# Kernel optimization log

Hardware: AMD Instinct MI355X
Metric: run time of the kernel (lower is better)

## Reference

```python
import jax, jax.numpy as jnp
import numpy as np

N, NFEAT, NHID1, NHID2 = 16384, 128, 128, 64

def setup_inputs() -> dict:
    key = jax.random.key(0)
    k1, k2, k3, k4 = jax.random.split(key, 4)
    feature = jax.random.normal(k1, (N, NFEAT), dtype=jnp.float32)
    # dense (row-normalized) adjacency surrogate
    adj = jax.random.uniform(k2, (N, N), dtype=jnp.float32) / N
    W1 = jax.random.normal(k3, (NFEAT, NHID1), dtype=jnp.float32) / np.sqrt(NFEAT)
    b1 = jnp.zeros((NHID1,), dtype=jnp.float32)
    W2 = jax.random.normal(k4, (NHID1, NHID2), dtype=jnp.float32) / np.sqrt(NHID1)
    b2 = jnp.zeros((NHID2,), dtype=jnp.float32)
    return {"feature": feature, "adj": adj, "W1": W1, "b1": b1, "W2": W2, "b2": b2}

def reference(feature, adj, W1, b1, W2, b2):
    # layer 1: support = X@W1; agg = A@support; relu
    h = jax.nn.relu(adj @ (feature @ W1) + b1)
    # dropout is identity in eval mode
    # layer 2
    out = adj @ (h @ W2) + b2
    return out
```

## Files before the change

kernel.cpp:

```cpp
#include <hip/hip_runtime.h>
#include <stdint.h>

typedef float  f32x4  __attribute__((ext_vector_type(4)));
typedef short  short8 __attribute__((ext_vector_type(8)));
typedef __bf16 bf16x8 __attribute__((ext_vector_type(8)));

__device__ __forceinline__ unsigned short f2bf(float f) {
    unsigned u = __builtin_bit_cast(unsigned, f);
    unsigned r = u + 0x7fffu + ((u >> 16) & 1u);
    return (unsigned short)(r >> 16);
}

__device__ __forceinline__ short8 cvt8(f32x4 a, f32x4 b) {
    short8 r;
    r[0] = (short)f2bf(a[0]); r[1] = (short)f2bf(a[1]);
    r[2] = (short)f2bf(a[2]); r[3] = (short)f2bf(a[3]);
    r[4] = (short)f2bf(b[0]); r[5] = (short)f2bf(b[1]);
    r[6] = (short)f2bf(b[2]); r[7] = (short)f2bf(b[3]);
    return r;
}

typedef const __attribute__((address_space(1))) void* gas_p;
typedef __attribute__((address_space(3))) void*       las_p;
__device__ __forceinline__ void gld_lds16(const void* g, void* l) {
    __builtin_amdgcn_global_load_lds((gas_p)g, (las_p)l, 16, 0, 0);
}

__device__ __forceinline__ f32x4 mfma16(short8 a, short8 b, f32x4 c) {
    return __builtin_amdgcn_mfma_f32_16x16x32_bf16(
        __builtin_bit_cast(bf16x8, a), __builtin_bit_cast(bf16x8, b), c, 0, 0, 0);
}

template<int NMAT>
__global__ __launch_bounds__(256) void k_xw_t(const float* __restrict__ X,
                                              const float* __restrict__ W,
                                              short* __restrict__ St, int M) {
    constexpr int K   = 128;
    constexpr int NPT = NMAT / 4;
    __shared__ float Xs[64][129];
    __shared__ float Ws[K][NMAT];

    const int tid = threadIdx.x;
    const int m0  = blockIdx.x * 64;

    constexpr int WCH = K * NMAT / 4 / 256;
    #pragma unroll
    for (int j = 0; j < WCH; ++j) {
        int ch = tid + j * 256;
        ((float4*)Ws)[ch] = ((const float4*)W)[ch];
    }
    #pragma unroll
    for (int j = 0; j < 8; ++j) {
        int ch = tid + j * 256;
        int r = ch >> 5, c4 = ch & 31;
        float4 v = *(const float4*)(X + (size_t)(m0 + r) * K + c4 * 4);
        Xs[r][c4 * 4 + 0] = v.x; Xs[r][c4 * 4 + 1] = v.y;
        Xs[r][c4 * 4 + 2] = v.z; Xs[r][c4 * 4 + 3] = v.w;
    }
    __syncthreads();

    const int m  = tid & 63;
    const int n0 = (tid >> 6) * NPT;
    float acc[NPT];
    #pragma unroll
    for (int i = 0; i < NPT; ++i) acc[i] = 0.f;

    for (int k = 0; k < K; ++k) {
        float x = Xs[m][k];
        #pragma unroll
        for (int i = 0; i < NPT; i += 4) {
            float4 w = *(const float4*)&Ws[k][n0 + i];
            acc[i + 0] += x * w.x; acc[i + 1] += x * w.y;
            acc[i + 2] += x * w.z; acc[i + 3] += x * w.w;
        }
    }
    #pragma unroll
    for (int i = 0; i < NPT; ++i)
        St[(size_t)(n0 + i) * M + m0 + m] = (short)f2bf(acc[i]);
}

template<int BN, bool RELU>
__global__ __launch_bounds__(128, 1) void k_adj_gemm(const float* __restrict__ A,
                                                     const short* __restrict__ Bt,
                                                     const float* __restrict__ bias,
                                                     float* __restrict__ out,
                                                     int M, int K) {
    constexpr int BM    = 32, BK = 64;
    constexpr int NF    = BN / 16;
    constexpr int BTILE = BN * BK * 2;
    constexpr int BCH   = BTILE / (128 * 16);
    constexpr int VMCNT = BCH + 8;

    __shared__ short Bs[2][BN * 64];

    const int tid  = threadIdx.x;
    const int wave = tid >> 6, lane = tid & 63;
    const int lr   = lane & 15, lk = lane >> 4;
    const int row_g = blockIdx.x * BM + wave * 16 + lr;

    const char* Abase = (const char*)A + (size_t)row_g * K * 4 + lk * 32;

    const int offs0 = (lk * 16)        ^ ((lr & 7) << 4);
    const int offs1 = (64 + lk * 16)   ^ ((lr & 7) << 4);

    f32x4 acc[NF];
    #pragma unroll
    for (int n = 0; n < NF; ++n) acc[n] = (f32x4)0.f;

    f32x4 a0[4], a1[4];
    const int NT = K / BK;

#define STAGE_B(BUF, KT)                                                        \
    {                                                                           \
        _Pragma("unroll")                                                       \
        for (int j = 0; j < BCH; ++j) {                                         \
            int o = (tid + j * 128) * 16;          \
            int r = o >> 7, w = o & 127;                                        \
            const char* src = (const char*)Bt + (size_t)r * (K * 2)             \
                              + (size_t)(KT) * 128 + (w ^ ((r & 7) << 4));      \
            gld_lds16(src, (char*)&Bs[BUF][0] + o);                             \
        }                                                                       \
    }

#define LOAD_A(SLOT, KT)                                                        \
    {                                                                           \
        const char* p = Abase + (size_t)(KT) * 256;                             \
        SLOT[0] = *(const f32x4*)(p);                                           \
        SLOT[1] = *(const f32x4*)(p + 16);                                      \
        SLOT[2] = *(const f32x4*)(p + 128);                                     \
        SLOT[3] = *(const f32x4*)(p + 144);                                     \
    }

    LOAD_A(a0, 0)
    STAGE_B(0, 0)
    LOAD_A(a1, 1)

#define ITER(KT, SA, CUR, NXT)                                                  \
    {                                                                           \
               \
        { int ktn = (KT) + 1 < NT ? (KT) + 1 : NT - 1; STAGE_B(NXT, ktn) }      \
        __builtin_amdgcn_sched_barrier(0);                                      \
             \
        short8 fa0 = cvt8(SA[0], SA[1]);                                        \
        short8 fa1 = cvt8(SA[2], SA[3]);                                        \
                                             \
        { int kta = (KT) + 2 < NT ? (KT) + 2 : NT - 1; LOAD_A(SA, kta) }        \
        __builtin_amdgcn_sched_barrier(0);                                      \
                              \
        asm volatile("s_waitcnt vmcnt(%0)" :: "i"(VMCNT) : "memory");           \
        __builtin_amdgcn_s_barrier();                                           \
        __builtin_amdgcn_sched_barrier(0);                                      \
                                      \
        _Pragma("unroll")                                                       \
        for (int n = 0; n < NF; ++n) {                                          \
            short8 b0 = *(const short8*)((const char*)&Bs[CUR][0]               \
                                         + n * 2048 + lr * 128 + offs0);        \
            acc[n] = mfma16(fa0, b0, acc[n]);                                   \
            short8 b1 = *(const short8*)((const char*)&Bs[CUR][0]               \
                                         + n * 2048 + lr * 128 + offs1);        \
            acc[n] = mfma16(fa1, b1, acc[n]);                                   \
        }                                                                       \
        __builtin_amdgcn_sched_barrier(0);                                      \
        __builtin_amdgcn_s_barrier();         \
    }

    for (int g = 0; g < NT / 2; ++g) {
        ITER(2 * g,     a0, 0, 1)
        ITER(2 * g + 1, a1, 1, 0)
    }
#undef ITER
#undef LOAD_A
#undef STAGE_B

    #pragma unroll
    for (int n = 0; n < NF; ++n) {
        int col = n * 16 + lr;
        float bv = bias[col];
        #pragma unroll
        for (int j = 0; j < 4; ++j) {
            int row = blockIdx.x * BM + wave * 16 + lk * 4 + j;
            float v = acc[n][j] + bv;
            if (RELU) v = fmaxf(v, 0.f);
            out[(size_t)row * BN + col] = v;
        }
    }
}

extern "C" void kernel_launch(void* const* d_in, const int* in_sizes, int n_in,
                              void* d_out, int out_size, void* d_ws, size_t ws_size,
                              hipStream_t stream) {
    const int N = 16384, NH1 = 128, NH2 = 64;
    const float* feature = (const float*)d_in[0];
    const float* adj     = (const float*)d_in[1];
    const float* W1      = (const float*)d_in[2];
    const float* b1      = (const float*)d_in[3];
    const float* W2      = (const float*)d_in[4];
    const float* b2      = (const float*)d_in[5];

    short* S1t = (short*)d_ws;
    float* h   = (float*)((char*)d_ws + (4u << 20));
    short* S2t = (short*)((char*)d_ws + (12u << 20));

    k_xw_t<NH1><<<N / 64, 256, 0, stream>>>(feature, W1, S1t, N);
    k_adj_gemm<NH1, true ><<<N / 32, 128, 0, stream>>>(adj, S1t, b1, h, N, N);
    k_xw_t<NH2><<<N / 64, 256, 0, stream>>>(h, W2, S2t, N);
    k_adj_gemm<NH2, false><<<N / 32, 128, 0, stream>>>(adj, S2t, b2, (float*)d_out, N, N);
    (void)in_sizes; (void)n_in; (void)out_size; (void)ws_size;
}
```

Before: 539.1 us.

## Use 64-row blocks with triple-buffered B tiles and one barrier per step

The adjacency GEMM now runs 256-thread blocks covering 64 rows, so each staged B tile is shared by four waves instead of two, which halves B traffic per row. B staging moves to a three-buffer LDS ring. That lets the trailing barrier go, leaving a single barrier per k-step, and the loop is unrolled six ways with a hard-coded trip count. The risks are more LDS per block, occupancy hints that may not hold, and a loop count fixed at K=16384, which breaks other sizes.

Result: no change. 533.5 us (-1.0%).

```diff
diff --git a/kernel.cpp b/kernel.cpp
--- a/kernel.cpp
+++ b/kernel.cpp
@@ -80,28 +80,29 @@
 }
 
 template<int BN, bool RELU>
-__global__ __launch_bounds__(128, 1) void k_adj_gemm(const float* __restrict__ A,
+__global__ __launch_bounds__(256, 2) void k_adj_gemm(const float* __restrict__ A,
                                                      const short* __restrict__ Bt,
                                                      const float* __restrict__ bias,
                                                      float* __restrict__ out,
                                                      int M, int K) {
-    constexpr int BM    = 32, BK = 64;
+    constexpr int BM    = 64, BK = 64;
     constexpr int NF    = BN / 16;
-    constexpr int BTILE = BN * BK * 2;
-    constexpr int BCH   = BTILE / (128 * 16);
-    constexpr int VMCNT = BCH + 8;
-
-    __shared__ short Bs[2][BN * 64];
+    constexpr int BCH   = BN * BK * 2 / (256 * 16);
+    constexpr int VMCNT = BCH + 4;
+
+    __shared__ short Bs[3][BN * 64];
 
     const int tid  = threadIdx.x;
     const int wave = tid >> 6, lane = tid & 63;
     const int lr   = lane & 15, lk = lane >> 4;
-    const int row_g = blockIdx.x * BM + wave * 16 + lr;
+    const int row0 = blockIdx.x * BM;
+    const int row_g = row0 + wave * 16 + lr;
 
     const char* Abase = (const char*)A + (size_t)row_g * K * 4 + lk * 32;
 
-    const int offs0 = (lk * 16)        ^ ((lr & 7) << 4);
-    const int offs1 = (64 + lk * 16)   ^ ((lr & 7) << 4);
+    const int key   = (lr & 7) << 4;
+    const int offs0 = (lk * 16) ^ key;
+    const int offs1 = (64 + lk * 16) ^ key;
 
     f32x4 acc[NF];
     #pragma unroll
@@ -109,18 +110,6 @@
 
     f32x4 a0[4], a1[4];
     const int NT = K / BK;
-
-#define STAGE_B(BUF, KT)                                                        \
-    {                                                                           \
-        _Pragma("unroll")                                                       \
-        for (int j = 0; j < BCH; ++j) {                                         \
-            int o = (tid + j * 128) * 16;          \
-            int r = o >> 7, w = o & 127;                                        \
-            const char* src = (const char*)Bt + (size_t)r * (K * 2)             \
-                              + (size_t)(KT) * 128 + (w ^ ((r & 7) << 4));      \
-            gld_lds16(src, (char*)&Bs[BUF][0] + o);                             \
-        }                                                                       \
-    }
 
 #define LOAD_A(SLOT, KT)                                                        \
     {                                                                           \
@@ -130,44 +119,60 @@
         SLOT[2] = *(const f32x4*)(p + 128);                                     \
         SLOT[3] = *(const f32x4*)(p + 144);                                     \
     }
+#define STAGE_B(BUF, KT)                                                        \
+    {                                                                           \
+        _Pragma("unroll")                                                       \
+        for (int j = 0; j < BCH; ++j) {                                         \
+            int o = (tid + j * 256) * 16;          \
+            int r = o >> 7, w = o & 127;                                        \
+            const char* src = (const char*)Bt + (size_t)r * (K * 2)             \
+                              + (size_t)(KT) * 128 + (w ^ ((r & 7) << 4));      \
+            gld_lds16(src, (char*)&Bs[BUF][0] + o);                             \
+        }                                                                       \
+    }
 
     LOAD_A(a0, 0)
+    LOAD_A(a1, 1)
     STAGE_B(0, 0)
-    LOAD_A(a1, 1)
-
-#define ITER(KT, SA, CUR, NXT)                                                  \
+
+#define ITER(KT, SA, CB, NB)                                                    \
     {                                                                           \
-               \
-        { int ktn = (KT) + 1 < NT ? (KT) + 1 : NT - 1; STAGE_B(NXT, ktn) }      \
-        __builtin_amdgcn_sched_barrier(0);                                      \
-             \
+           \
         short8 fa0 = cvt8(SA[0], SA[1]);                                        \
         short8 fa1 = cvt8(SA[2], SA[3]);                                        \
-                                             \
+            \
         { int kta = (KT) + 2 < NT ? (KT) + 2 : NT - 1; LOAD_A(SA, kta) }        \
+        { int ktn = (KT) + 1 < NT ? (KT) + 1 : NT - 1; STAGE_B(NB, ktn) }       \
         __builtin_amdgcn_sched_barrier(0);                                      \
-                              \
+                     \
         asm volatile("s_waitcnt vmcnt(%0)" :: "i"(VMCNT) : "memory");           \
-        __builtin_amdgcn_s_barrier();                                           \
+        __builtin_amdgcn_s_barrier();                     \
         __builtin_amdgcn_sched_barrier(0);                                      \
-                                      \
+                                       \
         _Pragma("unroll")                                                       \
         for (int n = 0; n < NF; ++n) {                                          \
-            short8 b0 = *(const short8*)((const char*)&Bs[CUR][0]               \
+            short8 b0 = *(const short8*)((const char*)&Bs[CB][0]                \
                                          + n * 2048 + lr * 128 + offs0);        \
             acc[n] = mfma16(fa0, b0, acc[n]);                                   \
-            short8 b1 = *(const short8*)((const char*)&Bs[CUR][0]               \
+            short8 b1 = *(const short8*)((const char*)&Bs[CB][0]                \
                                          + n * 2048 + lr * 128 + offs1);        \
             acc[n] = mfma16(fa1, b1, acc[n]);                                   \
         }                                                                       \
-        __builtin_amdgcn_sched_barrier(0);                                      \
-        __builtin_amdgcn_s_barrier();         \
-    }
-
-    for (int g = 0; g < NT / 2; ++g) {
-        ITER(2 * g,     a0, 0, 1)
-        ITER(2 * g + 1, a1, 1, 0)
-    }
+    }
+
+    for (int g = 0; g < 42; ++g) {
+        int t = g * 6;
+        ITER(t + 0, a0, 0, 1)
+        ITER(t + 1, a1, 1, 2)
+        ITER(t + 2, a0, 2, 0)
+        ITER(t + 3, a1, 0, 1)
+        ITER(t + 4, a0, 1, 2)
+        ITER(t + 5, a1, 2, 0)
+    }
+    ITER(252, a0, 0, 1)
+    ITER(253, a1, 1, 2)
+    ITER(254, a0, 2, 0)
+    ITER(255, a1, 0, 1)
 #undef ITER
 #undef LOAD_A
 #undef STAGE_B
@@ -178,7 +183,7 @@
         float bv = bias[col];
         #pragma unroll
         for (int j = 0; j < 4; ++j) {
-            int row = blockIdx.x * BM + wave * 16 + lk * 4 + j;
+            int row = row0 + wave * 16 + lk * 4 + j;
             float v = acc[n][j] + bv;
             if (RELU) v = fmaxf(v, 0.f);
             out[(size_t)row * BN + col] = v;
@@ -202,8 +207,8 @@
     short* S2t = (short*)((char*)d_ws + (12u << 20));
 
     k_xw_t<NH1><<<N / 64, 256, 0, stream>>>(feature, W1, S1t, N);
-    k_adj_gemm<NH1, true ><<<N / 32, 128, 0, stream>>>(adj, S1t, b1, h, N, N);
+    k_adj_gemm<NH1, true ><<<N / 64, 256, 0, stream>>>(adj, S1t, b1, h, N, N);
     k_xw_t<NH2><<<N / 64, 256, 0, stream>>>(h, W2, S2t, N);
-    k_adj_gemm<NH2, false><<<N / 32, 128, 0, stream>>>(adj, S2t, b2, (float*)d_out, N, N);
+    k_adj_gemm<NH2, false><<<N / 64, 256, 0, stream>>>(adj, S2t, b2, (float*)d_out, N, N);
     (void)in_sizes; (void)n_in; (void)out_size; (void)ws_size;
 }
```
